# Performance work log

Measured on AMD Instinct MI355X. Metric: run time of the kernel, lower is better.

Reference implementation:

```python
import jax, jax.numpy as jnp
import numpy as np

N = 8192        # number of nodes (dense adjacency)
IN_DIM = 128    # GCN in_dim
OUT_DIM = 128   # GCN out_dim
MASK_THRESH = 0.8
NEG_INF = 1e9


def setup_inputs() -> dict:
    key = jax.random.key(0)
    kA, kX, kW = jax.random.split(key, 3)
    A = jax.random.uniform(kA, (N, N), dtype=jnp.float32)
    X = jax.random.normal(kX, (N, IN_DIM), dtype=jnp.float32)
    # nn.Linear(in_dim, out_dim): weight [out_dim, in_dim], bias [out_dim]
    W = jax.random.normal(kW, (OUT_DIM, IN_DIM), dtype=jnp.float32) * (1.0 / np.sqrt(IN_DIM))
    b = jnp.zeros((OUT_DIM,), dtype=jnp.float32)
    return {"A": A, "X": X, "W": W, "b": b}


def reference(A, X, W, b):
    # GCN.forward: A_norm = softmax(A - 1e9 * (A <= 0.8), axis=-1)
    # out = leaky_relu(A_norm @ Linear(X))   (relu=True path)
    logits = A - NEG_INF * (A <= MASK_THRESH).astype(A.dtype)   # [N, N]
    A_norm = jax.nn.softmax(logits, axis=-1)                     # row-wise softmax
    XW = X @ W.T + b                                             # [N, OUT_DIM]
    return jax.nn.leaky_relu(A_norm @ XW, negative_slope=0.01)   # [N, OUT_DIM]
```

## Files before the change

kernel.cpp:

```cpp
#include <hip/hip_runtime.h>
#include <hip/hip_bf16.h>

#define N_NODES 8192
#define DIM 128
#define MASK_THRESH 0.8f
#define ROWS 32
#define RB (N_NODES / ROWS)
#define KSTEP 64

using f32x4  = __attribute__((ext_vector_type(4))) float;
using bf16x8 = __attribute__((ext_vector_type(8))) short;

static __device__ __forceinline__ short f2bf(float f) {
    unsigned u = __builtin_bit_cast(unsigned, f);
    u += 0x7fffu + ((u >> 16) & 1u);
    return (short)(u >> 16);
}

static __device__ __forceinline__ void gload16(const void* gsrc, void* ldst) {
    __builtin_amdgcn_global_load_lds(
        (const __attribute__((address_space(1))) unsigned int*)gsrc,
        (__attribute__((address_space(3))) unsigned int*)ldst,
        16, 0, 0);
}

__global__ __launch_bounds__(256) void build_vf_kernel(
    const float* __restrict__ X, const float* __restrict__ W,
    const float* __restrict__ bias, short* __restrict__ Vf) {
    __shared__ float xs[32][128];
    const int jt = blockIdx.x * 32;
    for (int e = threadIdx.x; e < 32 * 128; e += 256) {
        xs[e >> 7][e & 127] = X[(size_t)(jt + (e >> 7)) * DIM + (e & 127)];
    }
    __syncthreads();
    const int d  = threadIdx.x & 127;
    const int jh = threadIdx.x >> 7;
    float bv = bias[d];
    float acc[16];
#pragma unroll
    for (int i = 0; i < 16; i++) acc[i] = bv;
    const float* wrow = W + (size_t)d * DIM;
    for (int k = 0; k < DIM; k += 4) {
        f32x4 wv = *(const f32x4*)(wrow + k);
#pragma unroll
        for (int i = 0; i < 16; i++) {
            f32x4 xv = *(const f32x4*)(&xs[jh * 16 + i][k]);
            acc[i] = fmaf(xv[0], wv[0], acc[i]);
            acc[i] = fmaf(xv[1], wv[1], acc[i]);
            acc[i] = fmaf(xv[2], wv[2], acc[i]);
            acc[i] = fmaf(xv[3], wv[3], acc[i]);
        }
    }
    bf16x8 o0, o1;
#pragma unroll
    for (int i = 0; i < 8; i++) { o0[i] = f2bf(acc[i]); o1[i] = f2bf(acc[8 + i]); }
    const int kb = jt >> 5;
    const int t  = d >> 4;
    short* base = Vf + ((size_t)(kb * 8 + t) * 64 + (d & 15) + 32 * jh) * 8;
    *(bf16x8*)(base)       = o0;
    *(bf16x8*)(base + 128) = o1;
}

template <int WRITE_PARTIAL>
__global__ __launch_bounds__(256, 3) void fused_kernel(
    const float* __restrict__ A, const short* __restrict__ Vf,
    float* __restrict__ dst, float* __restrict__ Zp, int kchunk, int S) {

    __shared__ __align__(16) float smem_a[2 * 32 * 64];
    __shared__ __align__(16) short smem_v[2 * 16 * 512];
    __shared__ float zs2[2][16];

    const int tid   = threadIdx.x;
    const int wid   = tid >> 6;
    const int lane  = tid & 63;
    const int row_a = lane & 15;
    const int kg    = lane >> 4;
    const int wr    = wid >> 1;
    const int wc    = wid & 1;
    const int rb    = blockIdx.x / S;
    const int chunk = blockIdx.x - rb * S;
    const int r0    = rb * ROWS;
    const int k0    = chunk * kchunk;
    const int nsteps = kchunk >> 6;

    const float* asrcA[2]; int adstA[2];
#pragma unroll
    for (int i = 0; i < 2; i++) {
        const int rowt = wid * 8 + i * 4 + (lane >> 4);
        asrcA[i] = A + (size_t)(r0 + rowt) * N_NODES + k0
                     + (((lane & 15) ^ (rowt & 15)) << 2);
        adstA[i] = (wid * 8 + i * 4) * 64;
    }
    const short* vsrcV = Vf + ((size_t)(k0 >> 5) * 8 + wid * 4) * 512 + lane * 8;
    const int vdst0 = wid * 4 * 512;

    f32x4 acc[4];
#pragma unroll
    for (int t = 0; t < 4; t++) acc[t] = (f32x4)0.0f;
    float zacc = 0.0f;

    auto stage = [&](int s, int b) {
#pragma unroll
        for (int i = 0; i < 2; i++)
            gload16(asrcA[i] + (size_t)s * KSTEP, smem_a + b * 2048 + adstA[i]);
#pragma unroll
        for (int j = 0; j < 4; j++)
            gload16(vsrcV + (size_t)s * 8192 + j * 512, smem_v + b * 8192 + vdst0 + j * 512);
    };

    auto compute = [&](const float* ab, const short* vb) {
        const int rL = wr * 16 + row_a;
#pragma unroll
        for (int kb = 0; kb < 2; kb++) {
            const int c0 = kb * 8 + kg * 2;
            const f32x4 av0 = *(const f32x4*)(ab + rL * 64 + (((c0 + 0) ^ row_a) << 2));
            const f32x4 av1 = *(const f32x4*)(ab + rL * 64 + (((c0 + 1) ^ row_a) << 2));
            float p[8];
#pragma unroll
            for (int i = 0; i < 4; i++) {
                p[i]     = (av0[i] > MASK_THRESH) ? __expf(av0[i]) : 0.0f;
                p[i + 4] = (av1[i] > MASK_THRESH) ? __expf(av1[i]) : 0.0f;
            }
            bf16x8 af;
#pragma unroll
            for (int i = 0; i < 8; i++) { zacc += p[i]; af[i] = f2bf(p[i]); }
#pragma unroll
            for (int t = 0; t < 4; t++) {
                const bf16x8 bv = *(const bf16x8*)(vb + (kb * 8 + wc * 4 + t) * 512 + lane * 8);
                acc[t] = __builtin_amdgcn_mfma_f32_16x16x32_bf16(af, bv, acc[t], 0, 0, 0);
            }
        }
    };

    stage(0, 0);
    stage(1, 1);

    for (int ks = 0; ks < nsteps - 1; ks++) {
        asm volatile("s_waitcnt vmcnt(6)\n\ts_barrier" ::: "memory");
        compute(smem_a + (ks & 1) * 2048, smem_v + (ks & 1) * 8192);
        asm volatile("s_barrier" ::: "memory");
        if (ks + 2 < nsteps) stage(ks + 2, ks & 1);
    }
    asm volatile("s_waitcnt vmcnt(0)\n\ts_barrier" ::: "memory");
    compute(smem_a + ((nsteps - 1) & 1) * 2048, smem_v + ((nsteps - 1) & 1) * 8192);

    zacc += __shfl_xor(zacc, 16);
    zacc += __shfl_xor(zacc, 32);
    if (wc == 0 && lane < 16) zs2[wr][lane] = zacc;
    __syncthreads();

    if (WRITE_PARTIAL) {
#pragma unroll
        for (int t = 0; t < 4; t++)
#pragma unroll
            for (int r = 0; r < 4; r++) {
                const int rl  = wr * 16 + kg * 4 + r;
                const int col = wc * 64 + t * 16 + row_a;
                dst[((size_t)chunk * N_NODES + r0 + rl) * DIM + col] = acc[t][r];
            }
        if (wc == 0 && lane < 16)
            Zp[(size_t)chunk * N_NODES + r0 + wr * 16 + lane] = zacc;
    } else {
#pragma unroll
        for (int t = 0; t < 4; t++)
#pragma unroll
            for (int r = 0; r < 4; r++) {
                const int rl  = wr * 16 + kg * 4 + r;
                const int col = wc * 64 + t * 16 + row_a;
                const float v = acc[t][r] / zs2[wr][kg * 4 + r];
                dst[(size_t)(r0 + rl) * DIM + col] = (v > 0.0f) ? v : 0.01f * v;
            }
    }
}

__global__ __launch_bounds__(256) void reduce_kernel(
    const float* __restrict__ num, const float* __restrict__ Zp,
    float* __restrict__ out, int S) {
    const size_t i4 = (size_t)blockIdx.x * 256 + threadIdx.x;
    const int r  = (int)(i4 >> 5);
    const int c4 = (int)(i4 & 31) * 4;
    f32x4 s = (f32x4)0.0f;
    float z = 0.0f;
    for (int p = 0; p < S; p++) {
        s += *(const f32x4*)(num + ((size_t)p * N_NODES + r) * DIM + c4);
        z += Zp[(size_t)p * N_NODES + r];
    }
    f32x4 o;
#pragma unroll
    for (int j = 0; j < 4; j++) {
        const float v = s[j] / z;
        o[j] = (v > 0.0f) ? v : 0.01f * v;
    }
    *(f32x4*)(out + (size_t)r * DIM + c4) = o;
}

extern "C" void kernel_launch(void* const* d_in, const int* in_sizes, int n_in,
                              void* d_out, int out_size, void* d_ws, size_t ws_size,
                              hipStream_t stream) {
    const float* A = (const float*)d_in[0];
    const float* X = (const float*)d_in[1];
    const float* W = (const float*)d_in[2];
    const float* b = (const float*)d_in[3];
    float* out = (float*)d_out;

    const size_t VF_BYTES = (size_t)DIM * N_NODES * 2;
    short* Vf = (short*)d_ws;
    build_vf_kernel<<<N_NODES / 32, 256, 0, stream>>>(X, W, b, Vf);

    const size_t per_split = ((size_t)N_NODES * DIM + N_NODES) * sizeof(float);
    int S = 1;
    for (int cand = 8; cand >= 1; cand >>= 1) {
        if (VF_BYTES + (size_t)cand * per_split <= ws_size) { S = cand; break; }
    }

    if (S >= 2) {
        float* num = (float*)((char*)d_ws + VF_BYTES);
        float* Zp  = num + (size_t)S * N_NODES * DIM;
        fused_kernel<1><<<RB * S, 256, 0, stream>>>(A, Vf, num, Zp, N_NODES / S, S);
        reduce_kernel<<<(N_NODES * DIM / 4) / 256, 256, 0, stream>>>(num, Zp, out, S);
    } else {
        fused_kernel<0><<<RB, 256, 0, stream>>>(A, Vf, out, nullptr, N_NODES, 1);
    }
}
```

Measured before the change: 118.5 us.

## Drop double-buffered LDS pipeline, read Vf directly from global, raise occupancy

Replaces the two-stage asynchronous LDS pipeline with a single A tile buffer loaded and waited on every step. The Vf operand now goes straight from global memory into registers instead of being staged in LDS. The launch bound moves from 3 to 8 blocks per SIMD hint, so more waves can be resident to hide latency. In exchange the kernel loses explicit load/compute overlap, adds two full barriers per step, and depends on cache hits for the repeated Vf reads.

```diff
diff --git a/kernel.cpp b/kernel.cpp
--- a/kernel.cpp
+++ b/kernel.cpp
@@ -62,12 +62,11 @@
 }
 
 template <int WRITE_PARTIAL>
-__global__ __launch_bounds__(256, 3) void fused_kernel(
+__global__ __launch_bounds__(256, 8) void fused_kernel(
     const float* __restrict__ A, const short* __restrict__ Vf,
     float* __restrict__ dst, float* __restrict__ Zp, int kchunk, int S) {
 
-    __shared__ __align__(16) float smem_a[2 * 32 * 64];
-    __shared__ __align__(16) short smem_v[2 * 16 * 512];
+    __shared__ __align__(16) float smem_a[32 * 64];
     __shared__ float zs2[2][16];
 
     const int tid   = threadIdx.x;
@@ -91,30 +90,26 @@
                      + (((lane & 15) ^ (rowt & 15)) << 2);
         adstA[i] = (wid * 8 + i * 4) * 64;
     }
-    const short* vsrcV = Vf + ((size_t)(k0 >> 5) * 8 + wid * 4) * 512 + lane * 8;
-    const int vdst0 = wid * 4 * 512;
 
     f32x4 acc[4];
 #pragma unroll
     for (int t = 0; t < 4; t++) acc[t] = (f32x4)0.0f;
     float zacc = 0.0f;
 
-    auto stage = [&](int s, int b) {
+    for (int ks = 0; ks < nsteps; ks++) {
+        __syncthreads();
 #pragma unroll
         for (int i = 0; i < 2; i++)
-            gload16(asrcA[i] + (size_t)s * KSTEP, smem_a + b * 2048 + adstA[i]);
-#pragma unroll
-        for (int j = 0; j < 4; j++)
-            gload16(vsrcV + (size_t)s * 8192 + j * 512, smem_v + b * 8192 + vdst0 + j * 512);
-    };
-
-    auto compute = [&](const float* ab, const short* vb) {
-        const int rL = wr * 16 + row_a;
+            gload16(asrcA[i] + (size_t)ks * KSTEP, smem_a + adstA[i]);
+        __syncthreads();
+
+        const int kbg = (k0 >> 5) + ks * 2;
+        const int rL  = wr * 16 + row_a;
 #pragma unroll
         for (int kb = 0; kb < 2; kb++) {
             const int c0 = kb * 8 + kg * 2;
-            const f32x4 av0 = *(const f32x4*)(ab + rL * 64 + (((c0 + 0) ^ row_a) << 2));
-            const f32x4 av1 = *(const f32x4*)(ab + rL * 64 + (((c0 + 1) ^ row_a) << 2));
+            const f32x4 av0 = *(const f32x4*)(smem_a + rL * 64 + (((c0 + 0) ^ row_a) << 2));
+            const f32x4 av1 = *(const f32x4*)(smem_a + rL * 64 + (((c0 + 1) ^ row_a) << 2));
             float p[8];
 #pragma unroll
             for (int i = 0; i < 4; i++) {
@@ -124,25 +119,14 @@
             bf16x8 af;
 #pragma unroll
             for (int i = 0; i < 8; i++) { zacc += p[i]; af[i] = f2bf(p[i]); }
+            const short* vfb = Vf + ((size_t)(kbg + kb) * 8 + wc * 4) * 512 + lane * 8;
 #pragma unroll
             for (int t = 0; t < 4; t++) {
-                const bf16x8 bv = *(const bf16x8*)(vb + (kb * 8 + wc * 4 + t) * 512 + lane * 8);
+                const bf16x8 bv = *(const bf16x8*)(vfb + t * 512);
                 acc[t] = __builtin_amdgcn_mfma_f32_16x16x32_bf16(af, bv, acc[t], 0, 0, 0);
             }
         }
-    };
-
-    stage(0, 0);
-    stage(1, 1);
-
-    for (int ks = 0; ks < nsteps - 1; ks++) {
-        asm volatile("s_waitcnt vmcnt(6)\n\ts_barrier" ::: "memory");
-        compute(smem_a + (ks & 1) * 2048, smem_v + (ks & 1) * 8192);
-        asm volatile("s_barrier" ::: "memory");
-        if (ks + 2 < nsteps) stage(ks + 2, ks & 1);
-    }
-    asm volatile("s_waitcnt vmcnt(0)\n\ts_barrier" ::: "memory");
-    compute(smem_a + ((nsteps - 1) & 1) * 2048, smem_v + ((nsteps - 1) & 1) * 8192);
+    }
 
     zacc += __shfl_xor(zacc, 16);
     zacc += __shfl_xor(zacc, 32);
```

Measured after the change: 127.8 us. 7.8% more time.
